# Optimization experiments

Hardware: AMD Instinct MI355X
Metric: run time of the kernel (lower is better)

## Reference

```python
import jax, jax.numpy as jnp
import numpy as np

D_MODEL = 1024
NUM_HEADS = 16
HEAD_DIM = D_MODEL // NUM_HEADS
SCALE = HEAD_DIM ** -0.5
BATCH = 4096
N_MODULES = 8


def setup_inputs() -> dict:
    key = jax.random.key(0)
    ks = jax.random.split(key, 7)
    s = 1.0 / np.sqrt(D_MODEL)
    return {
        "query": jax.random.normal(ks[0], (BATCH, D_MODEL), jnp.float32),
        "kv_stack": jax.random.normal(ks[1], (N_MODULES, BATCH, D_MODEL), jnp.float32),
        "Wq": jax.random.normal(ks[2], (D_MODEL, D_MODEL), jnp.float32) * s,
        "Wk": jax.random.normal(ks[3], (D_MODEL, D_MODEL), jnp.float32) * s,
        "Wv": jax.random.normal(ks[4], (D_MODEL, D_MODEL), jnp.float32) * s,
        "Wo": jax.random.normal(ks[5], (D_MODEL, D_MODEL), jnp.float32) * s,
        "bo": jnp.zeros((D_MODEL,), jnp.float32),
    }


def reference(query, kv_stack, Wq, Wk, Wv, Wo, bo):
    # query: [B, D]; kv_stack: [M, B, D] (stacked module representations)
    B = query.shape[0]
    M = kv_stack.shape[0]
    # projections (nn.Linear: x @ W.T), split into heads; seq_len == 1
    q = (query @ Wq.T).reshape(B, NUM_HEADS, HEAD_DIM)            # [B,H,hd]
    k = jnp.einsum("mbd,ed->mbe", kv_stack, Wk).reshape(M, B, NUM_HEADS, HEAD_DIM)
    v = jnp.einsum("mbd,ed->mbe", kv_stack, Wv).reshape(M, B, NUM_HEADS, HEAD_DIM)
    # scores over the single kv position: [M,B,H,1]
    scores = jnp.einsum("bhd,mbhd->mbh", q, k)[..., None] * SCALE
    attn_weights = jax.nn.softmax(scores, axis=-1)  # softmax over size-1 axis -> ones
    attn_output = attn_weights * v                   # [M,B,H,hd] (dropout is eval/no-op)
    attn_output = attn_output.reshape(M, B, D_MODEL)
    out = jnp.einsum("mbe,oe->mbo", attn_output, Wo) + bo + query  # residual per module
    return out  # [M, B, D] (stacked in kv order instead of the dict)
```

## Files before the change

kernel.cpp:

```cpp
#include <hip/hip_runtime.h>
#include <hip/hip_bf16.h>


typedef __attribute__((ext_vector_type(4))) float f32x4;
typedef __attribute__((ext_vector_type(8))) short short8;

#define D_MODEL 1024
#define BATCH   4096
#define M_ROWS  32768

__device__ __forceinline__ short f2bf(float f) {
    union { float f; unsigned u; } x; x.f = f;
    unsigned r = (x.u + 0x7fffu + ((x.u >> 16) & 1u)) >> 16;
    return (short)r;
}

__device__ __forceinline__ unsigned bfpk(float lo, float hi) {
    __hip_bfloat162 h = __float22bfloat162_rn(make_float2(lo, hi));
    unsigned u; __builtin_memcpy(&u, &h, 4); return u;
}

__device__ __forceinline__ short8 cvt8(float4 a, float4 b) {
    union { unsigned u[4]; short8 s; } r;
    r.u[0] = bfpk(a.x, a.y);
    r.u[1] = bfpk(a.z, a.w);
    r.u[2] = bfpk(b.x, b.y);
    r.u[3] = bfpk(b.z, b.w);
    return r.s;
}

__global__ __launch_bounds__(256) void fuse_w_kernel(
        const float* __restrict__ Wo, const float* __restrict__ Wv,
        short* __restrict__ Cw) {
    __shared__ __align__(16) short Ash[64][32];
    __shared__ __align__(16) short Bsh[64][32];
    const int t = threadIdx.x;
    const int lane = t & 63;
    const int w = t >> 6;
    const int wr = w >> 1, wc = w & 1;
    const int brow = blockIdx.y * 64;
    const int bcol = blockIdx.x * 64;

    f32x4 acc[2][2];
#pragma unroll
    for (int m = 0; m < 2; ++m)
#pragma unroll
        for (int n = 0; n < 2; ++n) acc[m][n] = (f32x4)(0.0f);

    for (int kt = 0; kt < 32; ++kt) {
        const float* ga = Wo + (size_t)(brow + (t >> 2)) * D_MODEL + kt * 32 + (t & 3) * 8;
        float4 a0 = *(const float4*)ga;
        float4 a1 = *(const float4*)(ga + 4);
        float4 bv[2];
#pragma unroll
        for (int j = 0; j < 2; ++j) {
            int lin = j * 256 + t;
            int e = lin >> 4, c4 = lin & 15;
            bv[j] = *(const float4*)(Wv + (size_t)(kt * 32 + e) * D_MODEL + bcol + c4 * 4);
        }
        *reinterpret_cast<short8*>(&Ash[t >> 2][(t & 3) * 8]) = cvt8(a0, a1);
#pragma unroll
        for (int j = 0; j < 2; ++j) {
            int lin = j * 256 + t;
            int e = lin >> 4, c4 = lin & 15;
            int d = c4 * 4;
            Bsh[d + 0][e] = f2bf(bv[j].x);
            Bsh[d + 1][e] = f2bf(bv[j].y);
            Bsh[d + 2][e] = f2bf(bv[j].z);
            Bsh[d + 3][e] = f2bf(bv[j].w);
        }
        __syncthreads();
        {
            const int r = lane & 15, q = lane >> 4;
            short8 af[2], bfr[2];
#pragma unroll
            for (int m = 0; m < 2; ++m)
                af[m] = *reinterpret_cast<const short8*>(&Ash[wr * 32 + m * 16 + r][q * 8]);
#pragma unroll
            for (int n = 0; n < 2; ++n)
                bfr[n] = *reinterpret_cast<const short8*>(&Bsh[wc * 32 + n * 16 + r][q * 8]);
#pragma unroll
            for (int m = 0; m < 2; ++m)
#pragma unroll
                for (int n = 0; n < 2; ++n)
                    acc[m][n] = __builtin_amdgcn_mfma_f32_16x16x32_bf16(
                        af[m], bfr[n], acc[m][n], 0, 0, 0);
        }
        __syncthreads();
    }

    const int r = lane & 15, q = lane >> 4;
#pragma unroll
    for (int m = 0; m < 2; ++m)
#pragma unroll
        for (int n = 0; n < 2; ++n)
#pragma unroll
            for (int j = 0; j < 4; ++j) {
                int o = brow + wr * 32 + m * 16 + q * 4 + j;
                int d = bcol + wc * 32 + n * 16 + r;
                Cw[(size_t)o * D_MODEL + d] = f2bf(acc[m][n][j]);
            }
}

__global__ __launch_bounds__(256, 4) void attn_gemm_kernel(
        const float* __restrict__ kv, const float* __restrict__ query,
        const short* __restrict__ Cw, const float* __restrict__ bo,
        float* __restrict__ out) {
    __shared__ __align__(16) float Afs[64][32];
    __shared__ __align__(16) short Bsh[128][32];
    const int t = threadIdx.x;
    const int lane = t & 63;
    const int w = t >> 6;
    const int wr = w >> 1, wc = w & 1;
    const int r = lane & 15, q = lane >> 4;

    const int L = blockIdx.x;
    const int x = L & 7, j5 = L >> 3;
    const int bx = j5 & 7;
    const int rt = (j5 >> 3) * 8 + x;
    const int brow = rt * 64;

    f32x4 acc[2][4];
#pragma unroll
    for (int m = 0; m < 2; ++m)
#pragma unroll
        for (int n = 0; n < 4; ++n) acc[m][n] = (f32x4)(0.0f);

    for (int kt = 0; kt < 32; ++kt) {
#pragma unroll
        for (int i = 0; i < 2; ++i) {
            int chunk = i * 256 + t;
            int rl = chunk >> 3, c = chunk & 7;
            int cg = c ^ (rl & 7);
            const float* g = kv + (size_t)(brow + rl) * D_MODEL + kt * 32 + cg * 4;
            __builtin_amdgcn_global_load_lds(
                (const __attribute__((address_space(1))) void*)g,
                (__attribute__((address_space(3))) void*)
                    ((char*)&Afs[0][0] + i * 4096 + w * 1024),
                16, 0, 0);
        }
#pragma unroll
        for (int i = 0; i < 2; ++i) {
            int chunk = i * 256 + t;
            int rl = chunk >> 2, c8 = chunk & 3;
            const short* g = Cw + (size_t)(bx * 128 + rl) * D_MODEL + kt * 32 + c8 * 8;
            __builtin_amdgcn_global_load_lds(
                (const __attribute__((address_space(1))) void*)g,
                (__attribute__((address_space(3))) void*)
                    ((char*)&Bsh[0][0] + i * 4096 + w * 1024),
                16, 0, 0);
        }
        __syncthreads();
        {
            short8 af[2], bfr[4];
#pragma unroll
            for (int m = 0; m < 2; ++m) {
                int rl = wr * 32 + m * 16 + r;
                int c0 = (2 * q) ^ (rl & 7);
                int c1 = (2 * q + 1) ^ (rl & 7);
                float4 lo = *(const float4*)&Afs[rl][c0 * 4];
                float4 hi = *(const float4*)&Afs[rl][c1 * 4];
                af[m] = cvt8(lo, hi);
            }
#pragma unroll
            for (int n = 0; n < 4; ++n) {
                int rl = wc * 64 + n * 16 + r;
                bfr[n] = *reinterpret_cast<const short8*>(&Bsh[rl][q * 8]);
            }
#pragma unroll
            for (int m = 0; m < 2; ++m)
#pragma unroll
                for (int n = 0; n < 4; ++n)
                    acc[m][n] = __builtin_amdgcn_mfma_f32_16x16x32_bf16(
                        af[m], bfr[n], acc[m][n], 0, 0, 0);
        }
        __syncthreads();
    }

#pragma unroll
    for (int n = 0; n < 4; ++n) {
        int o = bx * 128 + wc * 64 + n * 16 + r;
        float bov = bo[o];
#pragma unroll
        for (int m = 0; m < 2; ++m) {
            int gb = brow + wr * 32 + m * 16 + q * 4;
#pragma unroll
            for (int j = 0; j < 4; ++j) {
                int grow = gb + j;
                out[(size_t)grow * D_MODEL + o] =
                    acc[m][n][j] + bov +
                    query[(size_t)(grow & (BATCH - 1)) * D_MODEL + o];
            }
        }
    }
}

extern "C" void kernel_launch(void* const* d_in, const int* in_sizes, int n_in,
                              void* d_out, int out_size, void* d_ws, size_t ws_size,
                              hipStream_t stream) {
    int kv_i = 1, q_i = 0, bo_i = 6;
    int w_i[4] = {2, 3, 4, 5};
    int nw = 0;
    for (int i = 0; i < n_in; ++i) {
        long s = in_sizes[i];
        if (s == 33554432) kv_i = i;
        else if (s == 4194304) q_i = i;
        else if (s == 1024) bo_i = i;
        else if (s == 1048576 && nw < 4) w_i[nw++] = i;
    }
    const float* query = (const float*)d_in[q_i];
    const float* kv    = (const float*)d_in[kv_i];
    const float* Wv    = (const float*)d_in[w_i[2]];
    const float* Wo    = (const float*)d_in[w_i[3]];
    const float* bo    = (const float*)d_in[bo_i];
    short* Cw  = (short*)d_ws;
    float* out = (float*)d_out;

    fuse_w_kernel<<<dim3(16, 16), dim3(256), 0, stream>>>(Wo, Wv, Cw);
    attn_gemm_kernel<<<dim3(4096), dim3(256), 0, stream>>>(kv, query, Cw, bo, out);
}
```

Measured before the change: 198.1 us.

## Double-buffer LDS tiles and swizzle Cw layout in attention GEMM

```diff
diff --git a/kernel.cpp b/kernel.cpp
--- a/kernel.cpp
+++ b/kernel.cpp
@@ -106,8 +106,8 @@
         const float* __restrict__ kv, const float* __restrict__ query,
         const short* __restrict__ Cw, const float* __restrict__ bo,
         float* __restrict__ out) {
-    __shared__ __align__(16) float Afs[64][32];
-    __shared__ __align__(16) short Bsh[128][32];
+    __shared__ __align__(16) float Afs[2][64][32];
+    __shared__ __align__(16) short Bsh[2][128][32];
     const int t = threadIdx.x;
     const int lane = t & 63;
     const int w = t >> 6;
@@ -126,7 +126,7 @@
 #pragma unroll
         for (int n = 0; n < 4; ++n) acc[m][n] = (f32x4)(0.0f);
 
-    for (int kt = 0; kt < 32; ++kt) {
+    auto stage = [&](int kt, int buf) {
 #pragma unroll
         for (int i = 0; i < 2; ++i) {
             int chunk = i * 256 + t;
@@ -136,44 +136,53 @@
             __builtin_amdgcn_global_load_lds(
                 (const __attribute__((address_space(1))) void*)g,
                 (__attribute__((address_space(3))) void*)
-                    ((char*)&Afs[0][0] + i * 4096 + w * 1024),
+                    ((char*)&Afs[buf][0][0] + i * 4096 + w * 1024),
                 16, 0, 0);
         }
 #pragma unroll
         for (int i = 0; i < 2; ++i) {
             int chunk = i * 256 + t;
-            int rl = chunk >> 2, c8 = chunk & 3;
-            const short* g = Cw + (size_t)(bx * 128 + rl) * D_MODEL + kt * 32 + c8 * 8;
+            int rl = chunk >> 2, sc = chunk & 3;
+            int lc = sc ^ ((rl >> 1) & 3);
+            const short* g = Cw + (size_t)(bx * 128 + rl) * D_MODEL + kt * 32 + lc * 8;
             __builtin_amdgcn_global_load_lds(
                 (const __attribute__((address_space(1))) void*)g,
                 (__attribute__((address_space(3))) void*)
-                    ((char*)&Bsh[0][0] + i * 4096 + w * 1024),
+                    ((char*)&Bsh[buf][0][0] + i * 4096 + w * 1024),
                 16, 0, 0);
         }
-        __syncthreads();
-        {
-            short8 af[2], bfr[4];
-#pragma unroll
-            for (int m = 0; m < 2; ++m) {
-                int rl = wr * 32 + m * 16 + r;
-                int c0 = (2 * q) ^ (rl & 7);
-                int c1 = (2 * q + 1) ^ (rl & 7);
-                float4 lo = *(const float4*)&Afs[rl][c0 * 4];
-                float4 hi = *(const float4*)&Afs[rl][c1 * 4];
-                af[m] = cvt8(lo, hi);
-            }
-#pragma unroll
-            for (int n = 0; n < 4; ++n) {
-                int rl = wc * 64 + n * 16 + r;
-                bfr[n] = *reinterpret_cast<const short8*>(&Bsh[rl][q * 8]);
-            }
-#pragma unroll
-            for (int m = 0; m < 2; ++m)
-#pragma unroll
-                for (int n = 0; n < 4; ++n)
-                    acc[m][n] = __builtin_amdgcn_mfma_f32_16x16x32_bf16(
-                        af[m], bfr[n], acc[m][n], 0, 0, 0);
-        }
+    };
+    auto compute = [&](int buf) {
+        short8 af[2], bfr[4];
+#pragma unroll
+        for (int m = 0; m < 2; ++m) {
+            int rl = wr * 32 + m * 16 + r;
+            int c0 = (2 * q) ^ (rl & 7);
+            int c1 = (2 * q + 1) ^ (rl & 7);
+            float4 lo = *(const float4*)&Afs[buf][rl][c0 * 4];
+            float4 hi = *(const float4*)&Afs[buf][rl][c1 * 4];
+            af[m] = cvt8(lo, hi);
+        }
+#pragma unroll
+        for (int n = 0; n < 4; ++n) {
+            int rl = wc * 64 + n * 16 + r;
+            int sc = q ^ ((rl >> 1) & 3);
+            bfr[n] = *reinterpret_cast<const short8*>(&Bsh[buf][rl][sc * 8]);
+        }
+#pragma unroll
+        for (int m = 0; m < 2; ++m)
+#pragma unroll
+            for (int n = 0; n < 4; ++n)
+                acc[m][n] = __builtin_amdgcn_mfma_f32_16x16x32_bf16(
+                    af[m], bfr[n], acc[m][n], 0, 0, 0);
+    };
+
+    stage(0, 0);
+    __syncthreads();
+    for (int kt = 0; kt < 32; ++kt) {
+        const int cur = kt & 1;
+        if (kt < 31) stage(kt + 1, cur ^ 1);
+        compute(cur);
         __syncthreads();
     }
 
```

Result: slower. 211.1 us (+6.6%).
